# Performance work log

Measured on AMD Instinct MI355X. Metric: run time of the kernel, lower is better.

Reference implementation:

```python
import jax, jax.numpy as jnp
import numpy as np

B, T, C = 4, 2048, 2048
H, HS = 16, 128  # num_heads, head_size; H*HS == C


def setup_inputs() -> dict:
    key = jax.random.key(0)
    k1, k2, k3, k4 = jax.random.split(key, 4)
    x = jax.random.normal(k1, (B, T, C), dtype=jnp.float32)
    # nn.Linear weights are [out, in]; scale ~ kaiming-uniform-ish
    w_qkv = jax.random.normal(k2, (3 * C, C), dtype=jnp.float32) * (1.0 / np.sqrt(C))
    w_proj = jax.random.normal(k3, (C, C), dtype=jnp.float32) * (1.0 / np.sqrt(C))
    b_proj = jax.random.normal(k4, (C,), dtype=jnp.float32) * 0.01
    return {"x": x, "w_qkv": w_qkv, "w_proj": w_proj, "b_proj": b_proj}


def reference(x, w_qkv, w_proj, b_proj):
    Bq, Tq, Cq = x.shape
    qkv = jnp.einsum("btc,dc->btd", x, w_qkv)  # [B,T,3C]
    q, k, v = jnp.split(qkv, 3, axis=2)
    # [B,T,C] -> [B,H,T,hs]
    q = q.reshape(Bq, Tq, H, HS).transpose(0, 2, 1, 3)
    k = k.reshape(Bq, Tq, H, HS).transpose(0, 2, 1, 3)
    v = v.reshape(Bq, Tq, H, HS).transpose(0, 2, 1, 3)
    scale = 1.0 / np.sqrt(HS)
    scores = jnp.einsum("bhqd,bhkd->bhqk", q, k) * scale  # [B,H,T,T]
    causal = jnp.tril(jnp.ones((Tq, Tq), dtype=bool))
    scores = jnp.where(causal, scores, jnp.finfo(scores.dtype).min)
    attn = jax.nn.softmax(scores, axis=-1)
    out = jnp.einsum("bhqk,bhkd->bhqd", attn, v)  # [B,H,T,hs]
    out = out.transpose(0, 2, 1, 3).reshape(Bq, Tq, Cq)
    out = jnp.einsum("btc,dc->btd", out, w_proj) + b_proj
    return out
```

## Files before the change

kernel.cpp:

```cpp
#include <hip/hip_runtime.h>

#define Tq 2048
#define Cq 2048
#define Hn 16
#define HSz 128
#define Bq 4
#define SCALE_QK 0.08838834764831845f

typedef __bf16 bf16x8 __attribute__((ext_vector_type(8)));
typedef float f32x4 __attribute__((ext_vector_type(4)));
typedef unsigned short u16;
typedef u16 u16x4 __attribute__((ext_vector_type(4)));

__device__ __forceinline__ u16 f2bf(float f) {
  unsigned u = __builtin_bit_cast(unsigned, f);
  u += 0x7FFFu + ((u >> 16) & 1u);
  return (u16)(u >> 16);
}

__device__ __forceinline__ bf16x8 ld_frag(const void* p) {
  bf16x8 v; __builtin_memcpy(&v, p, 16); return v;
}

__device__ __forceinline__ void glds16(void* lds, const void* g) {
  __builtin_amdgcn_global_load_lds(
      (const __attribute__((address_space(1))) void*)g,
      (__attribute__((address_space(3))) void*)lds, 16, 0, 0);
}

__global__ void cvt_bf16(const float* __restrict__ in, u16* __restrict__ out, int n) {
  int i = (blockIdx.x * 256 + threadIdx.x) * 4;
  if (i >= n) return;
  f32x4 v; __builtin_memcpy(&v, in + i, 16);
  u16x4 o;
  o[0] = f2bf(v[0]); o[1] = f2bf(v[1]); o[2] = f2bf(v[2]); o[3] = f2bf(v[3]);
  __builtin_memcpy(out + i, &o, 8);
}


#define LDA(s, mh) do { \
  _Pragma("unroll") for (int mi2_ = 0; mi2_ < 4; ++mi2_) \
  _Pragma("unroll") for (int kk_ = 0; kk_ < 2; ++kk_) { \
    const int row_ = (mh)*128 + wm*64 + mi2_*16 + lr; \
    af[mi2_*2+kk_] = ld_frag(AsB + (s)*32768 + row_*128 + ((kk_*64 + lg*16) ^ swz)); \
  } } while(0)

#define LDB(s, nh, BF) do { \
  _Pragma("unroll") for (int nf2_ = 0; nf2_ < 2; ++nf2_) \
  _Pragma("unroll") for (int kk_ = 0; kk_ < 2; ++kk_) { \
    const int row_ = (nh)*128 + wn*32 + nf2_*16 + lr; \
    BF[nf2_*2+kk_] = ld_frag(BsB + (s)*32768 + row_*128 + ((kk_*64 + lg*16) ^ swz)); \
  } } while(0)

#define QUAD(mh, nh, BF) do { \
  _Pragma("unroll") for (int mi2_ = 0; mi2_ < 4; ++mi2_) \
  _Pragma("unroll") for (int nf2_ = 0; nf2_ < 2; ++nf2_) \
  _Pragma("unroll") for (int kk_ = 0; kk_ < 2; ++kk_) \
    acc[(mh)*4+mi2_][(nh)*2+nf2_] = __builtin_amdgcn_mfma_f32_16x16x32_bf16( \
        af[mi2_*2+kk_], BF[nf2_*2+kk_], acc[(mh)*4+mi2_][(nh)*2+nf2_], 0, 0, 0); \
  } while(0)

#define STAGE_A(s, mh, k0) do { \
    u16* dst_ = Asu + (s)*16384 + (mh)*8192; \
    const u16* sp_ = A + (size_t)(m0 + (mh)*64 + arow0) * K + (k0) + srcE; \
    glds16(dst_ + w*512, sp_); \
    glds16(dst_ + (8+w)*512, sp_ + (size_t)128 * K); \
  } while(0)

#define STAGE_B(s, nh, k0) do { \
    u16* dst_ = Bsu + (s)*16384 + (nh)*8192; \
    glds16(dst_ + w*512,     Bm + (size_t)(n0 + (nh)*32 + brow0) * K + (k0) + srcE); \
    glds16(dst_ + (8+w)*512, Bm + (size_t)(n0 + (nh)*32 + brow1) * K + (k0) + srcE); \
  } while(0)

#define SYNC_MFMA(...) do { \
    asm volatile("s_barrier" ::: "memory"); \
    __builtin_amdgcn_s_setprio(1); \
    __VA_ARGS__; \
    __builtin_amdgcn_s_setprio(0); \
    asm volatile("s_barrier" ::: "memory"); \
  } while(0)

#define FENCE(n) asm volatile("s_waitcnt vmcnt(" #n ")" ::: "memory")

template <int EPI>
__global__ __launch_bounds__(512)
void gemm256(const u16* __restrict__ A, const u16* __restrict__ Bm, int K,
             u16* __restrict__ qout, u16* __restrict__ kout, u16* __restrict__ vtout,
             float* __restrict__ fout, const float* __restrict__ bias) {
  __shared__ u16 As2[2 * 256 * 64];
  __shared__ u16 Bs2[2 * 256 * 64];
  const int tid = threadIdx.x;
  const int w = tid >> 6, l = tid & 63;
  const int wm = w >> 2, wn = w & 3;
  const int lr = l & 15, lg = l >> 4;
  const int swz = (lr & 7) << 4;

  const int nwg = gridDim.x * gridDim.y;
  int ow = blockIdx.y * gridDim.x + blockIdx.x;
  ow = (ow & 7) * (nwg >> 3) + (ow >> 3);
  const int bx = ow % gridDim.x, by = ow / gridDim.x;
  const int m0 = by * 256, n0 = bx * 256;

  const int r0 = w * 8 + (l >> 3);
  const int arow0 = r0;
  const int brow0 = (r0 >> 5) * 64 + (r0 & 31);
  const int brow1 = (((r0 + 64) >> 5) & 3) * 64 + (r0 & 31);
  const int srcE = ((l & 7) ^ (l >> 3)) << 3;

  u16* Asu = As2; u16* Bsu = Bs2;
  const char* AsB = (const char*)As2;
  const char* BsB = (const char*)Bs2;

  f32x4 acc[8][4];
  const f32x4 fz = {0.f, 0.f, 0.f, 0.f};
#pragma unroll
  for (int i = 0; i < 8; ++i)
#pragma unroll
    for (int j = 0; j < 4; ++j) acc[i][j] = fz;

  bf16x8 af[8], bf0[4], bf1[4];

  STAGE_A(0, 0, 0);  STAGE_B(0, 0, 0);  STAGE_B(0, 1, 0);
  STAGE_A(0, 1, 0);
  STAGE_A(1, 0, 64); STAGE_B(1, 0, 64); STAGE_B(1, 1, 64);
  FENCE(8);
  asm volatile("s_barrier" ::: "memory");

  const int NP = K >> 7;
#pragma unroll 1
  for (int t = 0; t < NP - 1; ++t) {
    const int kt = t << 7;
    const int kA = kt + 128;

    LDA(0, 0); LDB(0, 0, bf0); LDB(0, 1, bf1);
    STAGE_A(1, 1, kt + 64);
    FENCE(8);
    SYNC_MFMA(QUAD(0, 0, bf0); QUAD(0, 1, bf1));
    LDA(0, 1);
    STAGE_A(0, 0, kA); STAGE_B(0, 0, kA); STAGE_B(0, 1, kA);
    FENCE(8);
    SYNC_MFMA(QUAD(1, 1, bf1); QUAD(1, 0, bf0));
    LDA(1, 0); LDB(1, 0, bf0); LDB(1, 1, bf1);
    STAGE_A(0, 1, kA);
    FENCE(8);
    SYNC_MFMA(QUAD(0, 0, bf0); QUAD(0, 1, bf1));
    LDA(1, 1);
    STAGE_A(1, 0, kA + 64); STAGE_B(1, 0, kA + 64); STAGE_B(1, 1, kA + 64);
    FENCE(8);
    SYNC_MFMA(QUAD(1, 1, bf1); QUAD(1, 0, bf0));
  }

  {
    const int kt = (NP - 1) << 7;
    LDA(0, 0); LDB(0, 0, bf0); LDB(0, 1, bf1);
    STAGE_A(1, 1, kt + 64);
    FENCE(8);
    SYNC_MFMA(QUAD(0, 0, bf0); QUAD(0, 1, bf1));
    LDA(0, 1);
    FENCE(2);
    SYNC_MFMA(QUAD(1, 1, bf1); QUAD(1, 0, bf0));
    LDA(1, 0); LDB(1, 0, bf0); LDB(1, 1, bf1);
    FENCE(0);
    SYNC_MFMA(QUAD(0, 0, bf0); QUAD(0, 1, bf1));
    LDA(1, 1);
    SYNC_MFMA(QUAD(1, 1, bf1); QUAD(1, 0, bf0));
  }

  if constexpr (EPI == 0) {
#pragma unroll
    for (int mi = 0; mi < 8; ++mi) {
      const int trow = m0 + wm * 128 + mi * 16 + lg * 4;
      const int bb = trow >> 11, tt0 = trow & 2047;
#pragma unroll
      for (int nf = 0; nf < 4; ++nf) {
        const int d = n0 + wn * 64 + nf * 16 + lr;
        const int part = d >> 11;
        const int dd = d & 2047;
        const int hh = dd >> 7, hs = dd & 127;
        if (part == 2) {
          u16x4 pk;
          pk[0] = f2bf(acc[mi][nf][0]); pk[1] = f2bf(acc[mi][nf][1]);
          pk[2] = f2bf(acc[mi][nf][2]); pk[3] = f2bf(acc[mi][nf][3]);
          size_t off = ((size_t)(bb * Hn + hh) * HSz + hs) * Tq + tt0;
          __builtin_memcpy(&vtout[off], &pk, 8);
        } else {
          u16* dst = (part == 0) ? qout : kout;
#pragma unroll
          for (int rr = 0; rr < 4; ++rr) {
            size_t off = ((size_t)(bb * Hn + hh) * Tq + (tt0 + rr)) * HSz + hs;
            dst[off] = f2bf(acc[mi][nf][rr]);
          }
        }
      }
    }
  } else {
#pragma unroll
    for (int mi = 0; mi < 8; ++mi) {
      const int trow = m0 + wm * 128 + mi * 16 + lg * 4;
#pragma unroll
      for (int nf = 0; nf < 4; ++nf) {
        const int d = n0 + wn * 64 + nf * 16 + lr;
        const float bv = bias[d];
#pragma unroll
        for (int rr = 0; rr < 4; ++rr)
          fout[(size_t)(trow + rr) * Cq + d] = acc[mi][nf][rr] + bv;
      }
    }
  }
}

#define KVB 64
__global__ __launch_bounds__(256, 2)
void attn_fwd(const u16* __restrict__ qb, const u16* __restrict__ kb,
              const u16* __restrict__ vtb, u16* __restrict__ ob) {
  __shared__ u16 Ks[2 * KVB * HSz];
  __shared__ u16 Vs[2 * HSz * KVB];
  __shared__ u16 Ps[4 * 32 * 32];

  const int tid = threadIdx.x;
  const int w = tid >> 6, l = tid & 63;
  const int lr = l & 15, lg = l >> 4;
  const int bh = blockIdx.x, jj0 = blockIdx.y;
  const int b = bh >> 4, h = bh & 15;

  const u16* qp = qb + (size_t)bh * Tq * HSz;
  const u16* kp = kb + (size_t)bh * Tq * HSz;
  const u16* vp = vtb + (size_t)bh * HSz * Tq;

#pragma unroll 1
  for (int pass = 0; pass < 2; ++pass) {
    const int qt = pass ? (15 - jj0) : jj0;
    const int q0 = qt * 128;

    bf16x8 qf[2][4];
#pragma unroll
    for (int mi = 0; mi < 2; ++mi)
#pragma unroll
      for (int kk = 0; kk < 4; ++kk) {
        int row = q0 + w * 32 + mi * 16 + lr;
        qf[mi][kk] = ld_frag(qp + (size_t)row * HSz + kk * 32 + lg * 8);
      }

    const f32x4 fz = {0.f, 0.f, 0.f, 0.f};
    f32x4 o[2][8];
    float mrow[2][4], lrow[2][4];
#pragma unroll
    for (int mi = 0; mi < 2; ++mi) {
#pragma unroll
      for (int nj = 0; nj < 8; ++nj) o[mi][nj] = fz;
#pragma unroll
      for (int rr = 0; rr < 4; ++rr) { mrow[mi][rr] = -1e30f; lrow[mi][rr] = 0.f; }
    }

    const int nt = 2 * (qt + 1);

    auto stage = [&](int t, int buf) {
      const int kv0 = t * KVB;
      u16* Kb = &Ks[buf * (KVB * HSz)];
      u16* Vb = &Vs[buf * (HSz * KVB)];
#pragma unroll
      for (int i = 0; i < 4; ++i) {
        int c = w * 4 + i;
        {
          int r = c * 4 + lg;
          int cb = (lr * 16) ^ ((r & 7) << 4);
          glds16(&Kb[c * 512], (const char*)(kp + (size_t)(kv0 + r) * HSz) + cb);
        }
        {
          int r = c * 8 + (l >> 3);
          int cb = ((l & 7) * 16) ^ ((r & 7) << 4);
          glds16(&Vb[c * 512], (const char*)(vp + (size_t)r * Tq + kv0) + cb);
        }
      }
    };

    stage(0, 0);
#pragma unroll 1
    for (int t = 0; t < nt; ++t) {
      const int buf = t & 1;
      if (t + 1 < nt) {
        stage(t + 1, buf ^ 1);
        asm volatile("s_waitcnt vmcnt(8)\ns_barrier" ::: "memory");
      } else {
        asm volatile("s_waitcnt vmcnt(0)\ns_barrier" ::: "memory");
      }
      const u16* Ksb = &Ks[buf * (KVB * HSz)];
      const u16* Vsb = &Vs[buf * (HSz * KVB)];
      const int kv0 = t * KVB;

      f32x4 s[2][4];
#pragma unroll
      for (int mi = 0; mi < 2; ++mi)
#pragma unroll
        for (int nj = 0; nj < 4; ++nj) s[mi][nj] = fz;
#pragma unroll
      for (int kk = 0; kk < 4; ++kk) {
        bf16x8 kf[4];
#pragma unroll
        for (int nj = 0; nj < 4; ++nj) {
          int row = nj * 16 + lr;
          int cb = (kk * 64 + lg * 16) ^ ((row & 7) << 4);
          kf[nj] = ld_frag((const char*)Ksb + row * 256 + cb);
        }
        __builtin_amdgcn_s_setprio(1);
#pragma unroll
        for (int mi = 0; mi < 2; ++mi)
#pragma unroll
          for (int nj = 0; nj < 4; ++nj)
            s[mi][nj] = __builtin_amdgcn_mfma_f32_16x16x32_bf16(qf[mi][kk], kf[nj], s[mi][nj], 0, 0, 0);
        __builtin_amdgcn_s_setprio(0);
      }

      const bool diag = (t >= nt - 2);
      float corr[2][4];
      bool grew = false;
#pragma unroll
      for (int mi = 0; mi < 2; ++mi) {
#pragma unroll
        for (int rr = 0; rr < 4; ++rr) {
          const int qrow = q0 + w * 32 + mi * 16 + lg * 4 + rr;
          float pm = -1e30f;
#pragma unroll
          for (int nj = 0; nj < 4; ++nj) {
            float v = s[mi][nj][rr] * SCALE_QK;
            if (diag && (kv0 + nj * 16 + lr) > qrow) v = -1e30f;
            s[mi][nj][rr] = v;
            pm = fmaxf(pm, v);
          }
          pm = fmaxf(pm, __shfl_xor(pm, 1));
          pm = fmaxf(pm, __shfl_xor(pm, 2));
          pm = fmaxf(pm, __shfl_xor(pm, 4));
          pm = fmaxf(pm, __shfl_xor(pm, 8));
          float mo = mrow[mi][rr];
          float mn = fmaxf(mo, pm);
          corr[mi][rr] = __expf(mo - mn);
          grew |= (pm > mo);
          mrow[mi][rr] = mn;
          float rs = 0.f;
#pragma unroll
          for (int nj = 0; nj < 4; ++nj) {
            float p = __expf(s[mi][nj][rr] - mn);
            s[mi][nj][rr] = p;
            rs += p;
          }
          rs += __shfl_xor(rs, 1);
          rs += __shfl_xor(rs, 2);
          rs += __shfl_xor(rs, 4);
          rs += __shfl_xor(rs, 8);
          lrow[mi][rr] = lrow[mi][rr] * corr[mi][rr] + rs;
        }
      }
      if (__any(grew)) {
#pragma unroll
        for (int mi = 0; mi < 2; ++mi)
#pragma unroll
          for (int nj = 0; nj < 8; ++nj)
#pragma unroll
            for (int rr = 0; rr < 4; ++rr) o[mi][nj][rr] *= corr[mi][rr];
      }

      char* pw = (char*)Ps + w * 2048;
#pragma unroll
      for (int kk = 0; kk < 2; ++kk) {
#pragma unroll
        for (int mi = 0; mi < 2; ++mi)
#pragma unroll
          for (int jj = 0; jj < 2; ++jj) {
            int nj = kk * 2 + jj;
#pragma unroll
            for (int rr = 0; rr < 4; ++rr) {
              int prow = mi * 16 + lg * 4 + rr;
              int pcb = (jj * 16 + lr) * 2;
              *(u16*)(pw + ((prow * 64 + pcb) ^ ((prow & 7) << 4))) = f2bf(s[mi][nj][rr]);
            }
          }
        bf16x8 pa[2];
#pragma unroll
        for (int mi = 0; mi < 2; ++mi) {
          int prow = mi * 16 + lr;
          pa[mi] = ld_frag(pw + ((prow * 64 + lg * 16) ^ ((prow & 7) << 4)));
        }
        __builtin_amdgcn_s_setprio(1);
#pragma unroll
        for (int nj = 0; nj < 8; ++nj) {
          int vrow = nj * 16 + lr;
          int cb = (kk * 64 + lg * 16) ^ ((vrow & 7) << 4);
          bf16x8 vf = ld_frag((const char*)Vsb + vrow * 128 + cb);
#pragma unroll
          for (int mi = 0; mi < 2; ++mi)
            o[mi][nj] = __builtin_amdgcn_mfma_f32_16x16x32_bf16(pa[mi], vf, o[mi][nj], 0, 0, 0);
        }
        __builtin_amdgcn_s_setprio(0);
      }

      asm volatile("s_barrier" ::: "memory");
    }

#pragma unroll
    for (int mi = 0; mi < 2; ++mi)
#pragma unroll
      for (int rr = 0; rr < 4; ++rr) {
        int trow = q0 + w * 32 + mi * 16 + lg * 4 + rr;
        float inv = 1.f / lrow[mi][rr];
#pragma unroll
        for (int nj = 0; nj < 8; ++nj) {
          int d = nj * 16 + lr;
          ob[((size_t)b * Tq + trow) * Cq + h * HSz + d] = f2bf(o[mi][nj][rr] * inv);
        }
      }
  }
}

extern "C" void kernel_launch(void* const* d_in, const int* in_sizes, int n_in,
                              void* d_out, int out_size, void* d_ws, size_t ws_size,
                              hipStream_t stream) {
  const float* x = (const float*)d_in[0];
  const float* w_qkv = (const float*)d_in[1];
  const float* w_proj = (const float*)d_in[2];
  const float* b_proj = (const float*)d_in[3];
  float* out = (float*)d_out;

  char* ws = (char*)d_ws;
  u16* xb     = (u16*)(ws);
  u16* wqkvb  = (u16*)(ws + (size_t)33554432);
  u16* wprojb = (u16*)(ws + (size_t)58720256);
  u16* qbp    = (u16*)(ws + (size_t)67108864);
  u16* kbp    = (u16*)(ws + (size_t)100663296);
  u16* vtbp   = (u16*)(ws + (size_t)134217728);
  (void)in_sizes; (void)n_in; (void)out_size; (void)ws_size;

  cvt_bf16<<<16384, 256, 0, stream>>>(x, xb, 16777216);
  cvt_bf16<<<12288, 256, 0, stream>>>(w_qkv, wqkvb, 12582912);
  cvt_bf16<<<4096, 256, 0, stream>>>(w_proj, wprojb, 4194304);

  gemm256<0><<<dim3(24, 32), 512, 0, stream>>>(xb, wqkvb, 2048, qbp, kbp, vtbp, nullptr, nullptr);

  attn_fwd<<<dim3(64, 8), 256, 0, stream>>>(qbp, kbp, vtbp, xb);

  gemm256<1><<<dim3(8, 32), 512, 0, stream>>>(xb, wprojb, 2048, nullptr, nullptr, nullptr, out, b_proj);
}
```

Measured before the change: 465.9 us.

## Double-buffer LDS fragment registers to overlap ds_reads with MFMA in GEMM

```diff
diff --git a/kernel.cpp b/kernel.cpp
--- a/kernel.cpp
+++ b/kernel.cpp
@@ -38,11 +38,11 @@
 }
 
 
-#define LDA(s, mh) do { \
+#define LDA(s, mh, AF) do { \
   _Pragma("unroll") for (int mi2_ = 0; mi2_ < 4; ++mi2_) \
   _Pragma("unroll") for (int kk_ = 0; kk_ < 2; ++kk_) { \
     const int row_ = (mh)*128 + wm*64 + mi2_*16 + lr; \
-    af[mi2_*2+kk_] = ld_frag(AsB + (s)*32768 + row_*128 + ((kk_*64 + lg*16) ^ swz)); \
+    AF[mi2_*2+kk_] = ld_frag(AsB + (s)*32768 + row_*128 + ((kk_*64 + lg*16) ^ swz)); \
   } } while(0)
 
 #define LDB(s, nh, BF) do { \
@@ -52,12 +52,12 @@
     BF[nf2_*2+kk_] = ld_frag(BsB + (s)*32768 + row_*128 + ((kk_*64 + lg*16) ^ swz)); \
   } } while(0)
 
-#define QUAD(mh, nh, BF) do { \
+#define QUAD(mh, nh, AF, BF) do { \
   _Pragma("unroll") for (int mi2_ = 0; mi2_ < 4; ++mi2_) \
   _Pragma("unroll") for (int nf2_ = 0; nf2_ < 2; ++nf2_) \
   _Pragma("unroll") for (int kk_ = 0; kk_ < 2; ++kk_) \
     acc[(mh)*4+mi2_][(nh)*2+nf2_] = __builtin_amdgcn_mfma_f32_16x16x32_bf16( \
-        af[mi2_*2+kk_], BF[nf2_*2+kk_], acc[(mh)*4+mi2_][(nh)*2+nf2_], 0, 0, 0); \
+        AF[mi2_*2+kk_], BF[nf2_*2+kk_], acc[(mh)*4+mi2_][(nh)*2+nf2_], 0, 0, 0); \
   } while(0)
 
 #define STAGE_A(s, mh, k0) do { \
@@ -73,14 +73,13 @@
     glds16(dst_ + (8+w)*512, Bm + (size_t)(n0 + (nh)*32 + brow1) * K + (k0) + srcE); \
   } while(0)
 
-#define SYNC_MFMA(...) do { \
-    asm volatile("s_barrier" ::: "memory"); \
+#define MFMA_BLK(...) do { \
     __builtin_amdgcn_s_setprio(1); \
     __VA_ARGS__; \
     __builtin_amdgcn_s_setprio(0); \
-    asm volatile("s_barrier" ::: "memory"); \
   } while(0)
 
+#define BAR asm volatile("s_barrier" ::: "memory")
 #define FENCE(n) asm volatile("s_waitcnt vmcnt(" #n ")" ::: "memory")
 
 template <int EPI>
@@ -119,52 +118,57 @@
 #pragma unroll
     for (int j = 0; j < 4; ++j) acc[i][j] = fz;
 
-  bf16x8 af[8], bf0[4], bf1[4];
+  bf16x8 afA[8], afB[8], bX0[4], bX1[4], bY0[4], bY1[4];
 
   STAGE_A(0, 0, 0);  STAGE_B(0, 0, 0);  STAGE_B(0, 1, 0);
   STAGE_A(0, 1, 0);
   STAGE_A(1, 0, 64); STAGE_B(1, 0, 64); STAGE_B(1, 1, 64);
+  STAGE_A(1, 1, 64);
   FENCE(8);
-  asm volatile("s_barrier" ::: "memory");
+  BAR;
+  LDA(0, 0, afA); LDB(0, 0, bX0); LDB(0, 1, bX1);
 
   const int NP = K >> 7;
 #pragma unroll 1
   for (int t = 0; t < NP - 1; ++t) {
-    const int kt = t << 7;
-    const int kA = kt + 128;
-
-    LDA(0, 0); LDB(0, 0, bf0); LDB(0, 1, bf1);
-    STAGE_A(1, 1, kt + 64);
-    FENCE(8);
-    SYNC_MFMA(QUAD(0, 0, bf0); QUAD(0, 1, bf1));
-    LDA(0, 1);
+    const int kA = (t << 7) + 128;
+
+    LDA(0, 1, afB);
+    MFMA_BLK(QUAD(0, 0, afA, bX0); QUAD(0, 1, afA, bX1));
+    BAR;
     STAGE_A(0, 0, kA); STAGE_B(0, 0, kA); STAGE_B(0, 1, kA);
     FENCE(8);
-    SYNC_MFMA(QUAD(1, 1, bf1); QUAD(1, 0, bf0));
-    LDA(1, 0); LDB(1, 0, bf0); LDB(1, 1, bf1);
+    BAR;
+    LDA(1, 0, afA); LDB(1, 0, bY0); LDB(1, 1, bY1);
+    MFMA_BLK(QUAD(1, 1, afB, bX1); QUAD(1, 0, afB, bX0));
+    BAR;
     STAGE_A(0, 1, kA);
     FENCE(8);
-    SYNC_MFMA(QUAD(0, 0, bf0); QUAD(0, 1, bf1));
-    LDA(1, 1);
+    BAR;
+    LDA(1, 1, afB);
+    MFMA_BLK(QUAD(0, 0, afA, bY0); QUAD(0, 1, afA, bY1));
+    BAR;
     STAGE_A(1, 0, kA + 64); STAGE_B(1, 0, kA + 64); STAGE_B(1, 1, kA + 64);
     FENCE(8);
-    SYNC_MFMA(QUAD(1, 1, bf1); QUAD(1, 0, bf0));
+    BAR;
+    LDA(0, 0, afA); LDB(0, 0, bX0); LDB(0, 1, bX1);
+    MFMA_BLK(QUAD(1, 1, afB, bY1); QUAD(1, 0, afB, bY0));
+    BAR;
+    STAGE_A(1, 1, kA + 64);
+    FENCE(8);
+    BAR;
   }
 
   {
-    const int kt = (NP - 1) << 7;
-    LDA(0, 0); LDB(0, 0, bf0); LDB(0, 1, bf1);
-    STAGE_A(1, 1, kt + 64);
-    FENCE(8);
-    SYNC_MFMA(QUAD(0, 0, bf0); QUAD(0, 1, bf1));
-    LDA(0, 1);
-    FENCE(2);
-    SYNC_MFMA(QUAD(1, 1, bf1); QUAD(1, 0, bf0));
-    LDA(1, 0); LDB(1, 0, bf0); LDB(1, 1, bf1);
-    FENCE(0);
-    SYNC_MFMA(QUAD(0, 0, bf0); QUAD(0, 1, bf1));
-    LDA(1, 1);
-    SYNC_MFMA(QUAD(1, 1, bf1); QUAD(1, 0, bf0));
+    LDA(0, 1, afB);
+    MFMA_BLK(QUAD(0, 0, afA, bX0); QUAD(0, 1, afA, bX1));
+    BAR; FENCE(2); BAR;
+    LDA(1, 0, afA); LDB(1, 0, bY0); LDB(1, 1, bY1);
+    MFMA_BLK(QUAD(1, 1, afB, bX1); QUAD(1, 0, afB, bX0));
+    BAR; FENCE(0); BAR;
+    LDA(1, 1, afB);
+    MFMA_BLK(QUAD(0, 0, afA, bY0); QUAD(0, 1, afA, bY1));
+    MFMA_BLK(QUAD(1, 1, afB, bY1); QUAD(1, 0, afB, bY0));
   }
 
   if constexpr (EPI == 0) {
```

Measured after the change: 1.293 ms. 2.78x slower.
